# Kernel tuning notes

Measured on AMD Instinct MI355X. Metric: run time of the kernel, lower is better.

The kernel has to match this reference:

```python
import jax, jax.numpy as jnp
import numpy as np

D = 128  # d_pair
N = 512  # n_res
B = 1
EPS = 1e-5


def setup_inputs() -> dict:
    key = jax.random.key(0)
    ks = jax.random.split(key, 16)
    s = 0.02
    inp = {
        "pair": jax.random.normal(ks[0], (B, N, N, D), dtype=jnp.float32),
        "pair_mask": jnp.ones((B, N, N), dtype=jnp.float32),
        "ln_g": jnp.ones((D,), dtype=jnp.float32),
        "ln_b": jnp.zeros((D,), dtype=jnp.float32),
        "w_lp": jax.random.normal(ks[1], (D, D), dtype=jnp.float32) * s,
        "b_lp": jnp.zeros((D,), dtype=jnp.float32),
        "w_lg": jax.random.normal(ks[2], (D, D), dtype=jnp.float32) * s,
        "b_lg": jnp.zeros((D,), dtype=jnp.float32),
        "w_rp": jax.random.normal(ks[3], (D, D), dtype=jnp.float32) * s,
        "b_rp": jnp.zeros((D,), dtype=jnp.float32),
        "w_rg": jax.random.normal(ks[4], (D, D), dtype=jnp.float32) * s,
        "b_rg": jnp.zeros((D,), dtype=jnp.float32),
        "w_g": jax.random.normal(ks[5], (D, D), dtype=jnp.float32) * s,
        "b_g": jnp.zeros((D,), dtype=jnp.float32),
        "w_o": jax.random.normal(ks[6], (D, D), dtype=jnp.float32) * s,
        "b_o": jnp.zeros((D,), dtype=jnp.float32),
    }
    return inp


def _layer_norm(x, g, b):
    mu = jnp.mean(x, axis=-1, keepdims=True)
    var = jnp.mean(jnp.square(x - mu), axis=-1, keepdims=True)
    return (x - mu) * jax.lax.rsqrt(var + EPS) * g + b


def reference(pair, pair_mask, ln_g, ln_b, w_lp, b_lp, w_lg, b_lg,
              w_rp, b_rp, w_rg, b_rg, w_g, b_g, w_o, b_o):
    # [B,N,N,D] pair representation; outgoing triangle multiplication
    x = _layer_norm(pair, ln_g, ln_b)
    mask = pair_mask[..., None]  # [B,N,N,1]
    left = (x @ w_lp + b_lp) * jax.nn.sigmoid(x @ w_lg + b_lg) * mask
    right = (x @ w_rp + b_rp) * jax.nn.sigmoid(x @ w_rg + b_rg) * mask
    # outgoing: contract over j -> per-channel NxN matmul
    out = jnp.einsum('bijd,bjkd->bikd', left, right)
    out = out * jax.nn.sigmoid(x @ w_g + b_g)
    out = out @ w_o + b_o
    return out
```

## Files before the change

### kernel.cpp

```cpp
#include <hip/hip_runtime.h>

#define NN 512
#define DD 128
#define PP (NN*NN)

typedef __attribute__((ext_vector_type(8))) short short8;
typedef __attribute__((ext_vector_type(4))) float floatx4;
typedef __attribute__((ext_vector_type(4))) unsigned int uintx4;

__device__ __forceinline__ unsigned short f2bf(float f) {
  unsigned int u = __float_as_uint(f);
  u += 0x7fffu + ((u >> 16) & 1u);
  return (unsigned short)(u >> 16);
}
__device__ __forceinline__ unsigned int pkbf2(float lo, float hi) {
  unsigned int r;
  asm("v_cvt_pk_bf16_f32 %0, %1, %2" : "=v"(r) : "v"(lo), "v"(hi));
  return r;
}
__device__ __forceinline__ float sigm(float x) {
  return 1.f / (1.f + __expf(-x));
}

__device__ __forceinline__ void gload_lds16(const unsigned short* g, unsigned short* l) {
  __builtin_amdgcn_global_load_lds(
      (const __attribute__((address_space(1))) unsigned int*)g,
      (__attribute__((address_space(3))) unsigned int*)l, 16, 0, 0);
}

__global__ void k0_prep(const float* __restrict__ wlp, const float* __restrict__ wlg,
                        const float* __restrict__ wrp, const float* __restrict__ wrg,
                        const float* __restrict__ wg,  const float* __restrict__ wo,
                        unsigned short* __restrict__ wt) {
  const float* src[6] = {wlp, wlg, wrp, wrg, wg, wo};
  int m = blockIdx.y;
  int idx = blockIdx.x * 256 + threadIdx.x;
  int d = idx >> 7, e = idx & 127;
  wt[m * 16384 + e * 128 + d] = f2bf(src[m][d * 128 + e]);
}

__launch_bounds__(256, 4)
__global__ void k1a_ln(const float* __restrict__ pair,
                       const float* __restrict__ lng, const float* __restrict__ lnb,
                       unsigned short* __restrict__ xln) {
  const int t = threadIdx.x;
  const long p0 = (long)blockIdx.x << 7;
  const int r = t >> 1, h = t & 1;
  const float* row = pair + (p0 + r) * DD + h * 64;
  floatx4 v[16];
  float s = 0.f, s2 = 0.f;
  #pragma unroll
  for (int c = 0; c < 16; ++c) {
    v[c] = *(const floatx4*)(row + c * 4);
    s  += v[c].x + v[c].y + v[c].z + v[c].w;
    s2 += v[c].x * v[c].x + v[c].y * v[c].y + v[c].z * v[c].z + v[c].w * v[c].w;
  }
  s  += __shfl_xor(s, 1);
  s2 += __shfl_xor(s2, 1);
  float mu = s * (1.f / 128.f);
  float var = s2 * (1.f / 128.f) - mu * mu;
  float rs = rsqrtf(var + 1e-5f);
  unsigned short* orow = xln + (p0 + r) * DD + h * 64;
  #pragma unroll
  for (int c2 = 0; c2 < 8; ++c2) {
    floatx4 g0 = *(const floatx4*)(lng + h * 64 + c2 * 8);
    floatx4 g1 = *(const floatx4*)(lng + h * 64 + c2 * 8 + 4);
    floatx4 b0 = *(const floatx4*)(lnb + h * 64 + c2 * 8);
    floatx4 b1 = *(const floatx4*)(lnb + h * 64 + c2 * 8 + 4);
    floatx4 a = v[2 * c2], b = v[2 * c2 + 1];
    uintx4 u;
    u[0] = pkbf2((a.x - mu) * rs * g0.x + b0.x, (a.y - mu) * rs * g0.y + b0.y);
    u[1] = pkbf2((a.z - mu) * rs * g0.z + b0.z, (a.w - mu) * rs * g0.w + b0.w);
    u[2] = pkbf2((b.x - mu) * rs * g1.x + b1.x, (b.y - mu) * rs * g1.y + b1.y);
    u[3] = pkbf2((b.z - mu) * rs * g1.z + b1.z, (b.w - mu) * rs * g1.w + b1.w);
    *(uintx4*)(orow + c2 * 8) = u;
  }
}

__launch_bounds__(512, 4)
__global__ void k1b_proj(const unsigned short* __restrict__ xln,
                         const float* __restrict__ pmask,
                         const unsigned short* __restrict__ wt,
                         const float* __restrict__ b_lp, const float* __restrict__ b_lg,
                         const float* __restrict__ b_rp, const float* __restrict__ b_rg,
                         const float* __restrict__ b_g,
                         unsigned short* __restrict__ left_t,
                         unsigned short* __restrict__ right_bt,
                         unsigned short* __restrict__ gate_t) {
  __shared__ __align__(16) unsigned short Sm[17408];
  __shared__ float Mlds[128];
  unsigned short* Al = Sm;
  unsigned short* Bp = Sm + 4096;
  unsigned short* Bg = Sm + 8192;

  const int t = threadIdx.x;
  const int unit = blockIdx.y;
  const int q = blockIdx.x;

  int j0 = 0, kk = 0;
  long p0 = 0, soff;
  if (unit == 1) {
    j0 = (q >> 9) << 7; kk = q & 511;
    soff = (long)kk * NN + j0;
  } else {
    p0 = (long)q << 7;
    soff = p0;
  }
  auto arow = [&](int r) -> long {
    return (unit == 1) ? ((long)(j0 + r) * NN + kk) : (p0 + r);
  };

  if (unit < 2 && t < 128) Mlds[t] = pmask[arow(t)];

  const unsigned short* wA = wt + (unit == 0 ? 0 : unit == 1 ? 2 : 4) * 16384;
  const unsigned short* wB = wt + (unit == 0 ? 1 : 3) * 16384;

  const int lane = t & 63, w = t >> 6;
  const int ln = lane & 15, q8 = lane >> 4;
  const int wm = (w >> 2) << 6, we = (w & 3) << 5;
  const int sr = t >> 2, sc = t & 3;

  floatx4 aP[4][2] = {}, aG[4][2] = {};
  for (int kc = 0; kc < 4; ++kc) {
    gload_lds16(xln + arow(sr) * DD + kc * 32 + sc * 8, &Al[t * 8]);
    gload_lds16(wA + sr * 128 + kc * 32 + sc * 8,       &Bp[t * 8]);
    if (unit < 2)
      gload_lds16(wB + sr * 128 + kc * 32 + sc * 8,     &Bg[t * 8]);
    __syncthreads();
    short8 a[4];
    #pragma unroll
    for (int i = 0; i < 4; ++i)
      a[i] = *(const short8*)&Al[(wm + i * 16 + ln) * 32 + q8 * 8];
    #pragma unroll
    for (int j = 0; j < 2; ++j) {
      short8 bpv = *(const short8*)&Bp[(we + j * 16 + ln) * 32 + q8 * 8];
      #pragma unroll
      for (int i = 0; i < 4; ++i)
        aP[i][j] = __builtin_amdgcn_mfma_f32_16x16x32_bf16(a[i], bpv, aP[i][j], 0, 0, 0);
    }
    if (unit < 2) {
      #pragma unroll
      for (int j = 0; j < 2; ++j) {
        short8 bgv = *(const short8*)&Bg[(we + j * 16 + ln) * 32 + q8 * 8];
        #pragma unroll
        for (int i = 0; i < 4; ++i)
          aG[i][j] = __builtin_amdgcn_mfma_f32_16x16x32_bf16(a[i], bgv, aG[i][j], 0, 0, 0);
      }
    }
    __syncthreads();
  }

  unsigned short* mystg = Sm + w * 2176;
  if (unit < 2) {
    const float* bpp = (unit == 0) ? b_lp : b_rp;
    const float* bgg = (unit == 0) ? b_lg : b_rg;
    #pragma unroll
    for (int j = 0; j < 2; ++j) {
      int eg = we + j * 16 + ln;
      float bp = bpp[eg], bg = bgg[eg];
      #pragma unroll
      for (int i = 0; i < 4; ++i) {
        float vv[4];
        #pragma unroll
        for (int r = 0; r < 4; ++r) {
          int m = wm + i * 16 + q8 * 4 + r;
          vv[r] = (aP[i][j][r] + bp) * sigm(aG[i][j][r] + bg) * Mlds[m];
        }
        unsigned int* du = (unsigned int*)&mystg[(j * 16 + ln) * 68 + i * 16 + q8 * 4];
        du[0] = pkbf2(vv[0], vv[1]);
        du[1] = pkbf2(vv[2], vv[3]);
      }
    }
  } else {
    #pragma unroll
    for (int j = 0; j < 2; ++j) {
      int eg = we + j * 16 + ln;
      float bg = b_g[eg];
      #pragma unroll
      for (int i = 0; i < 4; ++i) {
        float vv[4];
        #pragma unroll
        for (int r = 0; r < 4; ++r)
          vv[r] = sigm(aP[i][j][r] + bg);
        unsigned int* du = (unsigned int*)&mystg[(j * 16 + ln) * 68 + i * 16 + q8 * 4];
        du[0] = pkbf2(vv[0], vv[1]);
        du[1] = pkbf2(vv[2], vv[3]);
      }
    }
  }

  unsigned short* dstbase = (unit == 0) ? left_t : (unit == 1 ? right_bt : gate_t);
  #pragma unroll
  for (int itr = 0; itr < 4; ++itr) {
    int row = itr * 8 + (lane >> 3);
    int c = lane & 7;
    short8 vv = *(const short8*)&mystg[row * 68 + c * 8];
    long eg = we + row;
    *(short8*)(dstbase + eg * PP + soff + wm + c * 8) = vv;
  }
}

__launch_bounds__(512, 4)
__global__ void k2_einsum(const unsigned short* __restrict__ left_t,
                          const unsigned short* __restrict__ right_bt,
                          unsigned short* __restrict__ tmpg) {
  __shared__ __align__(16) unsigned short Sm[128 * 132];
  unsigned short* Al = Sm;
  unsigned short* Bl = Sm + 128 * 32;
  unsigned short* Cl = Sm;
  const int t = threadIdx.x;
  const int d = blockIdx.y;
  const int i0 = (blockIdx.x >> 2) << 7;
  const int k0 = (blockIdx.x & 3) << 7;
  const unsigned short* Ag = left_t   + (long)d * PP;
  const unsigned short* Bg = right_bt + (long)d * PP;
  const int lane = t & 63, w = t >> 6;
  const int ln = lane & 15, q8 = lane >> 4;
  const int wm = (w >> 2) << 6, wn = (w & 3) << 5;
  const int sr = t >> 2, sc = t & 3;

  floatx4 acc[4][2] = {};
  for (int j0 = 0; j0 < NN; j0 += 32) {
    gload_lds16(Ag + (long)(i0 + sr) * NN + j0 + sc * 8, &Al[t * 8]);
    gload_lds16(Bg + (long)(k0 + sr) * NN + j0 + sc * 8, &Bl[t * 8]);
    __syncthreads();
    short8 a[4], b[2];
    #pragma unroll
    for (int i = 0; i < 4; ++i)
      a[i] = *(const short8*)&Al[(wm + i * 16 + ln) * 32 + q8 * 8];
    #pragma unroll
    for (int j = 0; j < 2; ++j)
      b[j] = *(const short8*)&Bl[(wn + j * 16 + ln) * 32 + q8 * 8];
    #pragma unroll
    for (int i = 0; i < 4; ++i)
      #pragma unroll
      for (int j = 0; j < 2; ++j)
        acc[i][j] = __builtin_amdgcn_mfma_f32_16x16x32_bf16(a[i], b[j], acc[i][j], 0, 0, 0);
    __syncthreads();
  }
  #pragma unroll
  for (int i = 0; i < 4; ++i)
    #pragma unroll
    for (int j = 0; j < 2; ++j) {
      int n = wn + j * 16 + ln;
      #pragma unroll
      for (int r = 0; r < 4; ++r)
        Cl[(wm + i * 16 + q8 * 4 + r) * 132 + n] = f2bf(acc[i][j][r]);
    }
  __syncthreads();
  unsigned short* Og = tmpg + (long)d * PP;
  #pragma unroll
  for (int it = 0; it < 4; ++it) {
    int flat = it * 512 + t;
    int m = flat >> 4, c = flat & 15;
    *(short8*)(Og + (long)(i0 + m) * NN + k0 + c * 8) = *(const short8*)&Cl[m * 132 + c * 8];
  }
}

__launch_bounds__(512, 4)
__global__ void k3_out(const unsigned short* __restrict__ tmpg,
                       const unsigned short* __restrict__ gate_t,
                       const unsigned short* __restrict__ wt,
                       const float* __restrict__ b_o,
                       float* __restrict__ out) {
  __shared__ __align__(16) unsigned short Tl[128 * 144];
  unsigned int* TlU = (unsigned int*)Tl;
  const int t = threadIdx.x;
  const long p0 = (long)blockIdx.x << 7;
  const unsigned short* wo = wt + 5 * 16384;

  #pragma unroll
  for (int it = 0; it < 2; ++it) {
    int flat = it * 512 + t;
    int rp = flat >> 4;
    int c  = flat & 15;
    const unsigned short* ra = tmpg   + (long)(2 * rp) * PP + p0 + c * 8;
    const unsigned short* ga = gate_t + (long)(2 * rp) * PP + p0 + c * 8;
    uintx4 xa = *(const uintx4*)ra;
    uintx4 xb = *(const uintx4*)(ra + PP);
    uintx4 ya = *(const uintx4*)ga;
    uintx4 yb = *(const uintx4*)(ga + PP);
    int sw = ((c & 7) << 3) ^ ((c >> 3) << 2);
    #pragma unroll
    for (int cc = 0; cc < 4; ++cc) {
      float pl = __uint_as_float(xa[cc] << 16) * __uint_as_float(ya[cc] << 16);
      float ph = __uint_as_float(xa[cc] & 0xffff0000u) * __uint_as_float(ya[cc] & 0xffff0000u);
      float ql = __uint_as_float(xb[cc] << 16) * __uint_as_float(yb[cc] << 16);
      float qh = __uint_as_float(xb[cc] & 0xffff0000u) * __uint_as_float(yb[cc] & 0xffff0000u);
      int p = c * 8 + 2 * cc;
      TlU[p * 72 + (rp ^ sw)]       = pkbf2(pl, ql);
      TlU[(p + 1) * 72 + (rp ^ sw)] = pkbf2(ph, qh);
    }
  }
  __syncthreads();

  const int lane = t & 63, w = t >> 6;
  const int ln = lane & 15, q8 = lane >> 4;
  const int wm = (w >> 2) << 6, wn = (w & 3) << 5;

  floatx4 acc[4][2] = {};
  #pragma unroll
  for (int ks = 0; ks < 4; ++ks) {
    short8 a[4], b[2];
    #pragma unroll
    for (int i = 0; i < 4; ++i) {
      int p = wm + i * 16 + ln;
      int swh = (((p >> 3) & 7) << 4) ^ (((p >> 6) & 1) << 3);
      a[i] = *(const short8*)&Tl[p * 144 + ((ks * 32 + q8 * 8) ^ swh)];
    }
    #pragma unroll
    for (int j = 0; j < 2; ++j)
      b[j] = *(const short8*)(wo + (wn + j * 16 + ln) * 128 + ks * 32 + q8 * 8);
    #pragma unroll
    for (int i = 0; i < 4; ++i)
      #pragma unroll
      for (int j = 0; j < 2; ++j)
        acc[i][j] = __builtin_amdgcn_mfma_f32_16x16x32_bf16(a[i], b[j], acc[i][j], 0, 0, 0);
  }
  #pragma unroll
  for (int j = 0; j < 2; ++j) {
    int eg = wn + j * 16 + ln;
    float bias = b_o[eg];
    #pragma unroll
    for (int i = 0; i < 4; ++i)
      #pragma unroll
      for (int r = 0; r < 4; ++r) {
        int m = wm + i * 16 + q8 * 4 + r;
        out[(p0 + m) * DD + eg] = acc[i][j][r] + bias;
      }
  }
}

extern "C" void kernel_launch(void* const* d_in, const int* in_sizes, int n_in,
                              void* d_out, int out_size, void* d_ws, size_t ws_size,
                              hipStream_t stream) {
  const float* pair = (const float*)d_in[0];
  const float* pmask = (const float*)d_in[1];
  const float* ln_g = (const float*)d_in[2];
  const float* ln_b = (const float*)d_in[3];
  const float* w_lp = (const float*)d_in[4];
  const float* b_lp = (const float*)d_in[5];
  const float* w_lg = (const float*)d_in[6];
  const float* b_lg = (const float*)d_in[7];
  const float* w_rp = (const float*)d_in[8];
  const float* b_rp = (const float*)d_in[9];
  const float* w_rg = (const float*)d_in[10];
  const float* b_rg = (const float*)d_in[11];
  const float* w_g  = (const float*)d_in[12];
  const float* b_g  = (const float*)d_in[13];
  const float* w_o  = (const float*)d_in[14];
  const float* b_o  = (const float*)d_in[15];
  float* out = (float*)d_out;

  char* ws = (char*)d_ws;
  unsigned short* wt       = (unsigned short*)ws;
  unsigned short* xln      = (unsigned short*)(ws + 196608);
  unsigned short* left_t   = xln      + (size_t)PP * DD;
  unsigned short* right_bt = left_t   + (size_t)PP * DD;
  unsigned short* gate_t   = right_bt + (size_t)PP * DD;
  unsigned short* tmpg     = xln;

  k0_prep<<<dim3(64, 6), 256, 0, stream>>>(w_lp, w_lg, w_rp, w_rg, w_g, w_o, wt);
  k1a_ln<<<dim3(2048), 256, 0, stream>>>(pair, ln_g, ln_b, xln);
  k1b_proj<<<dim3(2048, 3), 512, 0, stream>>>(xln, pmask, wt,
      b_lp, b_lg, b_rp, b_rg, b_g, left_t, right_bt, gate_t);
  k2_einsum<<<dim3(16, 128), 512, 0, stream>>>(left_t, right_bt, tmpg);
  k3_out<<<dim3(2048), 512, 0, stream>>>(tmpg, gate_t, wt, b_o, out);
}
```

Before: 518.2 us.

## Double-buffer LDS staging in projection and einsum kernels

```diff
diff --git a/kernel.cpp b/kernel.cpp
--- a/kernel.cpp
+++ b/kernel.cpp
@@ -87,11 +87,8 @@
                          unsigned short* __restrict__ left_t,
                          unsigned short* __restrict__ right_bt,
                          unsigned short* __restrict__ gate_t) {
-  __shared__ __align__(16) unsigned short Sm[17408];
+  __shared__ __align__(16) unsigned short Sm[24576];
   __shared__ float Mlds[128];
-  unsigned short* Al = Sm;
-  unsigned short* Bp = Sm + 4096;
-  unsigned short* Bg = Sm + 8192;
 
   const int t = threadIdx.x;
   const int unit = blockIdx.y;
@@ -120,13 +117,26 @@
   const int wm = (w >> 2) << 6, we = (w & 3) << 5;
   const int sr = t >> 2, sc = t & 3;
 
+  const long aBase = arow(sr) * DD + sc * 8;
+
+  auto STAGE = [&](int set, int kc) {
+    unsigned short* base = Sm + set * 12288;
+    gload_lds16(xln + aBase + kc * 32,            &base[t * 8]);
+    gload_lds16(wA + sr * 128 + kc * 32 + sc * 8, &base[4096 + t * 8]);
+    if (unit < 2)
+      gload_lds16(wB + sr * 128 + kc * 32 + sc * 8, &base[8192 + t * 8]);
+  };
+
   floatx4 aP[4][2] = {}, aG[4][2] = {};
+  STAGE(0, 0);
+  __syncthreads();
+  #pragma unroll
   for (int kc = 0; kc < 4; ++kc) {
-    gload_lds16(xln + arow(sr) * DD + kc * 32 + sc * 8, &Al[t * 8]);
-    gload_lds16(wA + sr * 128 + kc * 32 + sc * 8,       &Bp[t * 8]);
-    if (unit < 2)
-      gload_lds16(wB + sr * 128 + kc * 32 + sc * 8,     &Bg[t * 8]);
-    __syncthreads();
+    const int cur = kc & 1;
+    if (kc < 3) STAGE(cur ^ 1, kc + 1);
+    unsigned short* Al = Sm + cur * 12288;
+    unsigned short* Bp = Al + 4096;
+    unsigned short* Bg = Al + 8192;
     short8 a[4];
     #pragma unroll
     for (int i = 0; i < 4; ++i)
@@ -204,9 +214,7 @@
 __global__ void k2_einsum(const unsigned short* __restrict__ left_t,
                           const unsigned short* __restrict__ right_bt,
                           unsigned short* __restrict__ tmpg) {
-  __shared__ __align__(16) unsigned short Sm[128 * 132];
-  unsigned short* Al = Sm;
-  unsigned short* Bl = Sm + 128 * 32;
+  __shared__ __align__(16) unsigned short Sm[16896];
   unsigned short* Cl = Sm;
   const int t = threadIdx.x;
   const int d = blockIdx.y;
@@ -219,11 +227,22 @@
   const int wm = (w >> 2) << 6, wn = (w & 3) << 5;
   const int sr = t >> 2, sc = t & 3;
 
+  const long aBase = (long)(i0 + sr) * NN + sc * 8;
+  const long bBase = (long)(k0 + sr) * NN + sc * 8;
+
+  auto STAGE = [&](int set, int jj) {
+    gload_lds16(Ag + aBase + jj, &Sm[set * 8192 + t * 8]);
+    gload_lds16(Bg + bBase + jj, &Sm[set * 8192 + 4096 + t * 8]);
+  };
+
   floatx4 acc[4][2] = {};
-  for (int j0 = 0; j0 < NN; j0 += 32) {
-    gload_lds16(Ag + (long)(i0 + sr) * NN + j0 + sc * 8, &Al[t * 8]);
-    gload_lds16(Bg + (long)(k0 + sr) * NN + j0 + sc * 8, &Bl[t * 8]);
-    __syncthreads();
+  STAGE(0, 0);
+  __syncthreads();
+  for (int it = 0; it < 16; ++it) {
+    const int cur = it & 1;
+    if (it < 15) STAGE(cur ^ 1, (it + 1) * 32);
+    unsigned short* Al = Sm + cur * 8192;
+    unsigned short* Bl = Al + 4096;
     short8 a[4], b[2];
     #pragma unroll
     for (int i = 0; i < 4; ++i)
```

Measured after the change: 513.2 us. About the same (-1.0%).
